# Performance work log

Hardware: AMD Instinct MI355X
Metric: run time of the kernel (lower is better)

## Reference

```python
import jax, jax.numpy as jnp
import numpy as np
from jax import lax

H = 64
IN = 3

def _lstm_layer(x, Wih, Whh, bih, bhh, collect):
    # x: [B, T, in]; Wih: [4H, in]; Whh: [4H, H]. PyTorch gate order: i, f, g, o.
    B = x.shape[0]
    h0 = jnp.zeros((B, H), x.dtype)
    c0 = jnp.zeros((B, H), x.dtype)
    b = bih + bhh
    def step(carry, xt):
        h, c = carry
        gates = xt @ Wih.T + h @ Whh.T + b  # [B, 4H]
        i, f, g, o = jnp.split(gates, 4, axis=-1)
        i = jax.nn.sigmoid(i); f = jax.nn.sigmoid(f)
        g = jnp.tanh(g); o = jax.nn.sigmoid(o)
        c = f * c + i * g
        h = o * jnp.tanh(c)
        return (h, c), (h if collect else None)
    xs = jnp.swapaxes(x, 0, 1)  # [T, B, in]
    (h, c), hs = lax.scan(step, (h0, c0), xs)
    if collect:
        return jnp.swapaxes(hs, 0, 1)  # [B, T, H]
    return h  # [B, H]


def setup_inputs() -> dict:
    key = jax.random.key(0)
    ks = jax.random.split(key, 14)
    s = 1.0 / np.sqrt(H)
    def u(k, shape):
        return jax.random.uniform(k, shape, jnp.float32, -s, s)
    return {
        "x": jax.random.normal(ks[0], (4096, 512, IN), jnp.float32),
        "Wih0": u(ks[1], (4 * H, IN)), "Whh0": u(ks[2], (4 * H, H)),
        "bih0": u(ks[3], (4 * H,)), "bhh0": u(ks[4], (4 * H,)),
        "Wih1": u(ks[5], (4 * H, H)), "Whh1": u(ks[6], (4 * H, H)),
        "bih1": u(ks[7], (4 * H,)), "bhh1": u(ks[8], (4 * H,)),
        "Wc1": jax.random.normal(ks[9], (32, H), jnp.float32) * 0.1,
        "bc1": jnp.zeros((32,), jnp.float32),
        "Wc2": jax.random.normal(ks[10], (1, 32), jnp.float32) * 0.1,
        "bc2": jnp.zeros((1,), jnp.float32),
    }


def reference(x, Wih0, Whh0, bih0, bhh0, Wih1, Whh1, bih1, bhh1, Wc1, bc1, Wc2, bc2):
    # 2-layer LSTM (dropout inactive at inference); only last timestep of layer 2 is used.
    h1 = _lstm_layer(x, Wih0, Whh0, bih0, bhh0, collect=True)   # [B, T, H]
    last = _lstm_layer(h1, Wih1, Whh1, bih1, bhh1, collect=False)  # [B, H]
    hidden = jax.nn.relu(last @ Wc1.T + bc1)  # [B, 32]
    out = jax.nn.sigmoid(hidden @ Wc2.T + bc2)  # [B, 1]
    return out
```

## Files before the change

### kernel.cpp

```cpp
#include <hip/hip_runtime.h>

#define TSEQ   512
#define BATCH  4096
#define MROWS  16

typedef short bf16x8 __attribute__((ext_vector_type(8)));
typedef short bf16x4 __attribute__((ext_vector_type(4)));
typedef float f32x4  __attribute__((ext_vector_type(4)));
typedef float f32x2  __attribute__((ext_vector_type(2)));
typedef unsigned int u32x2 __attribute__((ext_vector_type(2)));

#define NL2E  (-1.44269504f)
#define P2L2E (2.88539008f)

__device__ __forceinline__ unsigned short f2bf(float f) {
    unsigned int u = __builtin_bit_cast(unsigned int, f);
    return (unsigned short)((u + 0x8000u) >> 16);
}

__device__ __forceinline__ f32x2 cellupd2(const f32x4 a, const f32x4 b, f32x2& C) {
    f32x2 ei = {__builtin_amdgcn_exp2f(a[0]), __builtin_amdgcn_exp2f(b[0])};
    f32x2 ef = {__builtin_amdgcn_exp2f(a[1]), __builtin_amdgcn_exp2f(b[1])};
    f32x2 eg = {__builtin_amdgcn_exp2f(a[2]), __builtin_amdgcn_exp2f(b[2])};
    f32x2 eo = {__builtin_amdgcn_exp2f(a[3]), __builtin_amdgcn_exp2f(b[3])};
    f32x2 A  = 1.f + ei;
    f32x2 G1 = eg + 1.f;
    f32x2 F  = 1.f + ef;
    f32x2 t  = A * G1;
    f32x2 G2 = eg * P2L2E + (NL2E * 2.f);
    f32x2 num = C * t + G2 * F;
    f32x2 den = t * F;
    f32x2 r  = {__builtin_amdgcn_rcpf(den.x), __builtin_amdgcn_rcpf(den.y)};
    f32x2 Cn = num * r;
    Cn.x = fminf(Cn.x, 126.f);
    Cn.y = fminf(Cn.y, 126.f);
    C = Cn;
    f32x2 ec = {__builtin_amdgcn_exp2f(Cn.x), __builtin_amdgcn_exp2f(Cn.y)};
    f32x2 B  = 1.f + eo;
    f32x2 hn = ec - 1.f;
    f32x2 hd = B * (ec + 1.f);
    f32x2 rr = {__builtin_amdgcn_rcpf(hd.x), __builtin_amdgcn_rcpf(hd.y)};
    return hn * rr;
}


__global__ __launch_bounds__(512, 2) void lstm2_kernel(
    const float* __restrict__ x,
    const float* __restrict__ Wih0, const float* __restrict__ Whh0,
    const float* __restrict__ bih0, const float* __restrict__ bhh0,
    const float* __restrict__ Wih1, const float* __restrict__ Whh1,
    const float* __restrict__ bih1, const float* __restrict__ bhh1,
    const float* __restrict__ Wc1,  const float* __restrict__ bc1,
    const float* __restrict__ Wc2,  const float* __restrict__ bc2,
    float* __restrict__ out)
{
    __shared__ __align__(16) unsigned short ring[2][MROWS * 64];
    __shared__ __align__(16) unsigned short h2s[2][MROWS * 64];
    __shared__ __align__(16) unsigned short xq[64][128];
    __shared__ float h2f[MROWS][65];
    __shared__ float hid[MROWS][33];

    const int tid  = threadIdx.x;
    const int wv   = tid >> 6;
    const int lane = tid & 63;
    const int col  = lane & 15;
    const int lg   = lane >> 4;
    const int b0   = blockIdx.x * MROWS;
    const int sw   = (col & 7) << 4;

    for (int i = tid; i < 1024; i += 512) {
        ((unsigned int*)ring)[i] = 0u;
        ((unsigned int*)h2s)[i]  = 0u;
    }

    const int xrow = tid >> 5;
    const int xt   = tid & 31;
    const float* xb = x + ((size_t)(b0 + xrow) * TSEQ + xt) * 3;
    float xr0 = xb[0], xr1 = xb[1], xr2 = xb[2];
    {
        bf16x8 xf = {(short)f2bf(xr0),(short)f2bf(xr1),(short)f2bf(xr2),0,0,0,0,0};
        *(bf16x8*)((char*)xq + (xt << 8) + ((xrow << 4) ^ ((xt & 7) << 4))) = xf;
    }
    xr0 = xb[96]; xr1 = xb[97]; xr2 = xb[98];
    __syncthreads();

    const int rd0 = (col * 128 +      lg * 16) ^ sw;
    const int rd1 = (col * 128 + 64 + lg * 16) ^ sw;

#define FLUSH(S) do { \
    if (((S) & 31) == 16 && (S) < 480) { \
        const int c1_ = ((S) >> 5) + 1; \
        const int t64_ = ((c1_ & 1) << 5) + xt; \
        bf16x8 xf_ = {(short)f2bf(xr0),(short)f2bf(xr1),(short)f2bf(xr2),0,0,0,0,0}; \
        *(bf16x8*)((char*)xq + (t64_ << 8) + ((xrow << 4) ^ ((xt & 7) << 4))) = xf_; \
        if (c1_ < 15) { const float* p_ = xb + (c1_ + 1) * 96; xr0 = p_[0]; xr1 = p_[1]; xr2 = p_[2]; } \
    } \
} while(0)

    if (wv < 4) {
        const int wq = wv;
        const int ga = col & 3;
        const float sca = (ga == 2) ? P2L2E : NL2E;
        bf16x8 Wf[4][3];
        f32x4 bia4[4];
#pragma unroll
        for (int tt = 0; tt < 4; ++tt) {
            const int n = ga * 64 + 16 * (col >> 2) + 4 * wq + tt;
#pragma unroll
            for (int f = 0; f < 3; ++f)
#pragma unroll
                for (int i = 0; i < 8; ++i) {
                    const int k = f * 32 + lg * 8 + i;
                    float v = 0.f;
                    if (k < 64)      v = Whh0[n * 64 + k];
                    else if (k < 67) v = Wih0[n * 3 + (k - 64)];
                    Wf[tt][f][i] = (short)f2bf(sca * v);
                }
#pragma unroll
            for (int r = 0; r < 4; ++r) {
                const int nb = r * 64 + 16 * lg + 4 * wq + tt;
                bia4[tt][r] = ((r == 2) ? P2L2E : NL2E) * (bih0[nb] + bhh0[nb]);
            }
        }
        const int hw = (col * 128 + 32 * lg + 8 * wq) ^ sw;
        f32x2 C01 = {0.f, 0.f};
        f32x2 C23 = {0.f, 0.f};

#define L1B(RI, WI, S) do { \
        const char* rb_ = (const char*)ring[RI]; \
        bf16x8 v0_ = *(const bf16x8*)(rb_ + rd0); \
        bf16x8 v1_ = *(const bf16x8*)(rb_ + rd1); \
        bf16x8 v2_ = {0,0,0,0,0,0,0,0}; \
        if (lg == 0) \
            v2_ = *(const bf16x8*)((const char*)xq + ((((S)&63)) << 8) + ((col << 4) ^ (((S)&7) << 4))); \
        f32x4 a0_ = __builtin_amdgcn_mfma_f32_16x16x32_bf16(Wf[0][0], v0_, bia4[0],0,0,0); \
        f32x4 a1_ = __builtin_amdgcn_mfma_f32_16x16x32_bf16(Wf[1][0], v0_, bia4[1],0,0,0); \
        f32x4 a2_ = __builtin_amdgcn_mfma_f32_16x16x32_bf16(Wf[2][0], v0_, bia4[2],0,0,0); \
        f32x4 a3_ = __builtin_amdgcn_mfma_f32_16x16x32_bf16(Wf[3][0], v0_, bia4[3],0,0,0); \
        a0_ = __builtin_amdgcn_mfma_f32_16x16x32_bf16(Wf[0][1], v1_, a0_,0,0,0); \
        a1_ = __builtin_amdgcn_mfma_f32_16x16x32_bf16(Wf[1][1], v1_, a1_,0,0,0); \
        a2_ = __builtin_amdgcn_mfma_f32_16x16x32_bf16(Wf[2][1], v1_, a2_,0,0,0); \
        a3_ = __builtin_amdgcn_mfma_f32_16x16x32_bf16(Wf[3][1], v1_, a3_,0,0,0); \
        a0_ = __builtin_amdgcn_mfma_f32_16x16x32_bf16(Wf[0][2], v2_, a0_,0,0,0); \
        a1_ = __builtin_amdgcn_mfma_f32_16x16x32_bf16(Wf[1][2], v2_, a1_,0,0,0); \
        a2_ = __builtin_amdgcn_mfma_f32_16x16x32_bf16(Wf[2][2], v2_, a2_,0,0,0); \
        a3_ = __builtin_amdgcn_mfma_f32_16x16x32_bf16(Wf[3][2], v2_, a3_,0,0,0); \
        f32x2 h01_ = cellupd2(a0_, a1_, C01); \
        f32x2 h23_ = cellupd2(a2_, a3_, C23); \
        unsigned int p0_, p1_; \
        asm("v_cvt_pk_bf16_f32 %0, %1, %2" : "=v"(p0_) : "v"(h01_.x), "v"(h01_.y)); \
        asm("v_cvt_pk_bf16_f32 %0, %1, %2" : "=v"(p1_) : "v"(h23_.x), "v"(h23_.y)); \
        u32x2 pk_ = {p0_, p1_}; \
        *(u32x2*)((char*)ring[WI] + hw) = pk_; \
    } while(0)

        L1B(1, 0, 0);
        __syncthreads();
#pragma unroll 1
        for (int m = 0; m < 255; ++m) {
            const int s1 = 2 * m + 1;
            L1B(0, 1, s1);
            __syncthreads();
            L1B(1, 0, s1 + 1);
            FLUSH(s1 + 1);
            __syncthreads();
        }
        L1B(0, 1, 511);
        __syncthreads();
        __syncthreads();
#undef L1B
    } else {
        const int wq = wv - 4;
        const int ga = col & 3;
        const float sca = (ga == 2) ? P2L2E : NL2E;
        bf16x8 Wf[4][4];
        f32x4 bia4[4];
#pragma unroll
        for (int tt = 0; tt < 4; ++tt) {
            const int n = ga * 64 + 16 * (col >> 2) + 4 * wq + tt;
#pragma unroll
            for (int f = 0; f < 4; ++f)
#pragma unroll
                for (int i = 0; i < 8; ++i) {
                    const int k = f * 32 + lg * 8 + i;
                    const float v = (k < 64) ? Wih1[n * 64 + k] : Whh1[n * 64 + (k - 64)];
                    Wf[tt][f][i] = (short)f2bf(sca * v);
                }
#pragma unroll
            for (int r = 0; r < 4; ++r) {
                const int nb = r * 64 + 16 * lg + 4 * wq + tt;
                bia4[tt][r] = ((r == 2) ? P2L2E : NL2E) * (bih1[nb] + bhh1[nb]);
            }
        }
        const int hw2 = (col * 128 + 32 * lg + 8 * wq) ^ sw;
        f32x2 C01 = {0.f, 0.f};
        f32x2 C23 = {0.f, 0.f};
        f32x2 hv01 = {0.f, 0.f};
        f32x2 hv23 = {0.f, 0.f};

#define L2B(RB, HR) do { \
        const char* rb_ = (const char*)ring[RB]; \
        const char* hp_ = (const char*)h2s[HR]; \
        bf16x8 v0_ = *(const bf16x8*)(rb_ + rd0); \
        bf16x8 v1_ = *(const bf16x8*)(rb_ + rd1); \
        bf16x8 v2_ = *(const bf16x8*)(hp_ + rd0); \
        bf16x8 v3_ = *(const bf16x8*)(hp_ + rd1); \
        f32x4 a0_ = __builtin_amdgcn_mfma_f32_16x16x32_bf16(Wf[0][0], v0_, bia4[0],0,0,0); \
        f32x4 a1_ = __builtin_amdgcn_mfma_f32_16x16x32_bf16(Wf[1][0], v0_, bia4[1],0,0,0); \
        f32x4 a2_ = __builtin_amdgcn_mfma_f32_16x16x32_bf16(Wf[2][0], v0_, bia4[2],0,0,0); \
        f32x4 a3_ = __builtin_amdgcn_mfma_f32_16x16x32_bf16(Wf[3][0], v0_, bia4[3],0,0,0); \
        a0_ = __builtin_amdgcn_mfma_f32_16x16x32_bf16(Wf[0][1], v1_, a0_,0,0,0); \
        a1_ = __builtin_amdgcn_mfma_f32_16x16x32_bf16(Wf[1][1], v1_, a1_,0,0,0); \
        a2_ = __builtin_amdgcn_mfma_f32_16x16x32_bf16(Wf[2][1], v1_, a2_,0,0,0); \
        a3_ = __builtin_amdgcn_mfma_f32_16x16x32_bf16(Wf[3][1], v1_, a3_,0,0,0); \
        a0_ = __builtin_amdgcn_mfma_f32_16x16x32_bf16(Wf[0][2], v2_, a0_,0,0,0); \
        a1_ = __builtin_amdgcn_mfma_f32_16x16x32_bf16(Wf[1][2], v2_, a1_,0,0,0); \
        a2_ = __builtin_amdgcn_mfma_f32_16x16x32_bf16(Wf[2][2], v2_, a2_,0,0,0); \
        a3_ = __builtin_amdgcn_mfma_f32_16x16x32_bf16(Wf[3][2], v2_, a3_,0,0,0); \
        a0_ = __builtin_amdgcn_mfma_f32_16x16x32_bf16(Wf[0][3], v3_, a0_,0,0,0); \
        a1_ = __builtin_amdgcn_mfma_f32_16x16x32_bf16(Wf[1][3], v3_, a1_,0,0,0); \
        a2_ = __builtin_amdgcn_mfma_f32_16x16x32_bf16(Wf[2][3], v3_, a2_,0,0,0); \
        a3_ = __builtin_amdgcn_mfma_f32_16x16x32_bf16(Wf[3][3], v3_, a3_,0,0,0); \
        hv01 = cellupd2(a0_, a1_, C01); \
        hv23 = cellupd2(a2_, a3_, C23); \
        unsigned int p0_, p1_; \
        asm("v_cvt_pk_bf16_f32 %0, %1, %2" : "=v"(p0_) : "v"(hv01.x), "v"(hv01.y)); \
        asm("v_cvt_pk_bf16_f32 %0, %1, %2" : "=v"(p1_) : "v"(hv23.x), "v"(hv23.y)); \
        u32x2 pk_ = {p0_, p1_}; \
        *(u32x2*)((char*)h2s[RB] + hw2) = pk_; \
    } while(0)

        __syncthreads();
#pragma unroll 1
        for (int m = 0; m < 255; ++m) {
            L2B(0, 1);
            __syncthreads();
            L2B(1, 0);
            FLUSH(2 * m + 2);
            __syncthreads();
        }
        L2B(0, 1);
        __syncthreads();
        L2B(1, 0);
        __syncthreads();
#undef L2B
        const int ub = 16 * lg + 4 * wq;
        h2f[col][ub + 0] = hv01.x;
        h2f[col][ub + 1] = hv01.y;
        h2f[col][ub + 2] = hv23.x;
        h2f[col][ub + 3] = hv23.y;
    }
    __syncthreads();

    {
        const int b = tid & 15, j = tid >> 4;
        float s = bc1[j];
#pragma unroll 8
        for (int k = 0; k < 64; ++k) s += Wc1[j * 64 + k] * h2f[b][k];
        hid[b][j] = fmaxf(s, 0.f);
    }
    __syncthreads();
    if (tid < 16) {
        float s = bc2[0];
#pragma unroll 8
        for (int k = 0; k < 32; ++k) s += Wc2[k] * hid[tid][k];
        float e = __builtin_amdgcn_exp2f(NL2E * s);
        out[b0 + tid] = __builtin_amdgcn_rcpf(1.f + e);
    }
}

extern "C" void kernel_launch(void* const* d_in, const int* in_sizes, int n_in,
                              void* d_out, int out_size, void* d_ws, size_t ws_size,
                              hipStream_t stream) {
    lstm2_kernel<<<BATCH / MROWS, 512, 0, stream>>>(
        (const float*)d_in[0],
        (const float*)d_in[1], (const float*)d_in[2],
        (const float*)d_in[3], (const float*)d_in[4],
        (const float*)d_in[5], (const float*)d_in[6],
        (const float*)d_in[7], (const float*)d_in[8],
        (const float*)d_in[9], (const float*)d_in[10],
        (const float*)d_in[11], (const float*)d_in[12],
        (float*)d_out);
}
```

Before: 309.3 us.

## Split each LSTM layer across eight waves with two gate tiles each

```diff
diff --git a/kernel.cpp b/kernel.cpp
--- a/kernel.cpp
+++ b/kernel.cpp
@@ -8,7 +8,6 @@
 typedef short bf16x4 __attribute__((ext_vector_type(4)));
 typedef float f32x4  __attribute__((ext_vector_type(4)));
 typedef float f32x2  __attribute__((ext_vector_type(2)));
-typedef unsigned int u32x2 __attribute__((ext_vector_type(2)));
 
 #define NL2E  (-1.44269504f)
 #define P2L2E (2.88539008f)
@@ -44,7 +43,7 @@
 }
 
 
-__global__ __launch_bounds__(512, 2) void lstm2_kernel(
+__global__ __launch_bounds__(1024, 4) void lstm2_kernel(
     const float* __restrict__ x,
     const float* __restrict__ Wih0, const float* __restrict__ Whh0,
     const float* __restrict__ bih0, const float* __restrict__ bhh0,
@@ -68,20 +67,19 @@
     const int b0   = blockIdx.x * MROWS;
     const int sw   = (col & 7) << 4;
 
-    for (int i = tid; i < 1024; i += 512) {
-        ((unsigned int*)ring)[i] = 0u;
-        ((unsigned int*)h2s)[i]  = 0u;
-    }
-
-    const int xrow = tid >> 5;
+    ((unsigned int*)ring)[tid] = 0u;
+    ((unsigned int*)h2s)[tid]  = 0u;
+
+    const int xrow = (tid >> 5) & 15;
     const int xt   = tid & 31;
     const float* xb = x + ((size_t)(b0 + xrow) * TSEQ + xt) * 3;
-    float xr0 = xb[0], xr1 = xb[1], xr2 = xb[2];
-    {
+    float xr0 = 0.f, xr1 = 0.f, xr2 = 0.f;
+    if (tid < 512) {
+        xr0 = xb[0]; xr1 = xb[1]; xr2 = xb[2];
         bf16x8 xf = {(short)f2bf(xr0),(short)f2bf(xr1),(short)f2bf(xr2),0,0,0,0,0};
         *(bf16x8*)((char*)xq + (xt << 8) + ((xrow << 4) ^ ((xt & 7) << 4))) = xf;
-    }
-    xr0 = xb[96]; xr1 = xb[97]; xr2 = xb[98];
+        xr0 = xb[96]; xr1 = xb[97]; xr2 = xb[98];
+    }
     __syncthreads();
 
     const int rd0 = (col * 128 +      lg * 16) ^ sw;
@@ -97,15 +95,15 @@
     } \
 } while(0)
 
-    if (wv < 4) {
+    if (wv < 8) {
         const int wq = wv;
         const int ga = col & 3;
         const float sca = (ga == 2) ? P2L2E : NL2E;
-        bf16x8 Wf[4][3];
-        f32x4 bia4[4];
-#pragma unroll
-        for (int tt = 0; tt < 4; ++tt) {
-            const int n = ga * 64 + 16 * (col >> 2) + 4 * wq + tt;
+        bf16x8 Wf[2][3];
+        f32x4 bia4[2];
+#pragma unroll
+        for (int tt = 0; tt < 2; ++tt) {
+            const int n = ga * 64 + 16 * (col >> 2) + 2 * wq + tt;
 #pragma unroll
             for (int f = 0; f < 3; ++f)
 #pragma unroll
@@ -118,13 +116,12 @@
                 }
 #pragma unroll
             for (int r = 0; r < 4; ++r) {
-                const int nb = r * 64 + 16 * lg + 4 * wq + tt;
+                const int nb = r * 64 + 16 * lg + 2 * wq + tt;
                 bia4[tt][r] = ((r == 2) ? P2L2E : NL2E) * (bih0[nb] + bhh0[nb]);
             }
         }
-        const int hw = (col * 128 + 32 * lg + 8 * wq) ^ sw;
+        const int hw = (col * 128 + 32 * lg + 4 * wq) ^ sw;
         f32x2 C01 = {0.f, 0.f};
-        f32x2 C23 = {0.f, 0.f};
 
 #define L1B(RI, WI, S) do { \
         const char* rb_ = (const char*)ring[RI]; \
@@ -135,23 +132,14 @@
             v2_ = *(const bf16x8*)((const char*)xq + ((((S)&63)) << 8) + ((col << 4) ^ (((S)&7) << 4))); \
         f32x4 a0_ = __builtin_amdgcn_mfma_f32_16x16x32_bf16(Wf[0][0], v0_, bia4[0],0,0,0); \
         f32x4 a1_ = __builtin_amdgcn_mfma_f32_16x16x32_bf16(Wf[1][0], v0_, bia4[1],0,0,0); \
-        f32x4 a2_ = __builtin_amdgcn_mfma_f32_16x16x32_bf16(Wf[2][0], v0_, bia4[2],0,0,0); \
-        f32x4 a3_ = __builtin_amdgcn_mfma_f32_16x16x32_bf16(Wf[3][0], v0_, bia4[3],0,0,0); \
         a0_ = __builtin_amdgcn_mfma_f32_16x16x32_bf16(Wf[0][1], v1_, a0_,0,0,0); \
         a1_ = __builtin_amdgcn_mfma_f32_16x16x32_bf16(Wf[1][1], v1_, a1_,0,0,0); \
-        a2_ = __builtin_amdgcn_mfma_f32_16x16x32_bf16(Wf[2][1], v1_, a2_,0,0,0); \
-        a3_ = __builtin_amdgcn_mfma_f32_16x16x32_bf16(Wf[3][1], v1_, a3_,0,0,0); \
         a0_ = __builtin_amdgcn_mfma_f32_16x16x32_bf16(Wf[0][2], v2_, a0_,0,0,0); \
         a1_ = __builtin_amdgcn_mfma_f32_16x16x32_bf16(Wf[1][2], v2_, a1_,0,0,0); \
-        a2_ = __builtin_amdgcn_mfma_f32_16x16x32_bf16(Wf[2][2], v2_, a2_,0,0,0); \
-        a3_ = __builtin_amdgcn_mfma_f32_16x16x32_bf16(Wf[3][2], v2_, a3_,0,0,0); \
         f32x2 h01_ = cellupd2(a0_, a1_, C01); \
-        f32x2 h23_ = cellupd2(a2_, a3_, C23); \
-        unsigned int p0_, p1_; \
+        unsigned int p0_; \
         asm("v_cvt_pk_bf16_f32 %0, %1, %2" : "=v"(p0_) : "v"(h01_.x), "v"(h01_.y)); \
-        asm("v_cvt_pk_bf16_f32 %0, %1, %2" : "=v"(p1_) : "v"(h23_.x), "v"(h23_.y)); \
-        u32x2 pk_ = {p0_, p1_}; \
-        *(u32x2*)((char*)ring[WI] + hw) = pk_; \
+        *(unsigned int*)((char*)ring[WI] + hw) = p0_; \
     } while(0)
 
         L1B(1, 0, 0);
@@ -170,14 +158,14 @@
         __syncthreads();
 #undef L1B
     } else {
-        const int wq = wv - 4;
+        const int wq = wv - 8;
         const int ga = col & 3;
         const float sca = (ga == 2) ? P2L2E : NL2E;
-        bf16x8 Wf[4][4];
-        f32x4 bia4[4];
-#pragma unroll
-        for (int tt = 0; tt < 4; ++tt) {
-            const int n = ga * 64 + 16 * (col >> 2) + 4 * wq + tt;
+        bf16x8 Wf[2][4];
+        f32x4 bia4[2];
+#pragma unroll
+        for (int tt = 0; tt < 2; ++tt) {
+            const int n = ga * 64 + 16 * (col >> 2) + 2 * wq + tt;
 #pragma unroll
             for (int f = 0; f < 4; ++f)
 #pragma unroll
@@ -188,15 +176,13 @@
                 }
 #pragma unroll
             for (int r = 0; r < 4; ++r) {
-                const int nb = r * 64 + 16 * lg + 4 * wq + tt;
+                const int nb = r * 64 + 16 * lg + 2 * wq + tt;
                 bia4[tt][r] = ((r == 2) ? P2L2E : NL2E) * (bih1[nb] + bhh1[nb]);
             }
         }
-        const int hw2 = (col * 128 + 32 * lg + 8 * wq) ^ sw;
+        const int hw2 = (col * 128 + 32 * lg + 4 * wq) ^ sw;
         f32x2 C01 = {0.f, 0.f};
-        f32x2 C23 = {0.f, 0.f};
         f32x2 hv01 = {0.f, 0.f};
-        f32x2 hv23 = {0.f, 0.f};
 
 #define L2B(RB, HR) do { \
         const char* rb_ = (const char*)ring[RB]; \
@@ -207,27 +193,16 @@
         bf16x8 v3_ = *(const bf16x8*)(hp_ + rd1); \
         f32x4 a0_ = __builtin_amdgcn_mfma_f32_16x16x32_bf16(Wf[0][0], v0_, bia4[0],0,0,0); \
         f32x4 a1_ = __builtin_amdgcn_mfma_f32_16x16x32_bf16(Wf[1][0], v0_, bia4[1],0,0,0); \
-        f32x4 a2_ = __builtin_amdgcn_mfma_f32_16x16x32_bf16(Wf[2][0], v0_, bia4[2],0,0,0); \
-        f32x4 a3_ = __builtin_amdgcn_mfma_f32_16x16x32_bf16(Wf[3][0], v0_, bia4[3],0,0,0); \
         a0_ = __builtin_amdgcn_mfma_f32_16x16x32_bf16(Wf[0][1], v1_, a0_,0,0,0); \
         a1_ = __builtin_amdgcn_mfma_f32_16x16x32_bf16(Wf[1][1], v1_, a1_,0,0,0); \
-        a2_ = __builtin_amdgcn_mfma_f32_16x16x32_bf16(Wf[2][1], v1_, a2_,0,0,0); \
-        a3_ = __builtin_amdgcn_mfma_f32_16x16x32_bf16(Wf[3][1], v1_, a3_,0,0,0); \
         a0_ = __builtin_amdgcn_mfma_f32_16x16x32_bf16(Wf[0][2], v2_, a0_,0,0,0); \
         a1_ = __builtin_amdgcn_mfma_f32_16x16x32_bf16(Wf[1][2], v2_, a1_,0,0,0); \
-        a2_ = __builtin_amdgcn_mfma_f32_16x16x32_bf16(Wf[2][2], v2_, a2_,0,0,0); \
-        a3_ = __builtin_amdgcn_mfma_f32_16x16x32_bf16(Wf[3][2], v2_, a3_,0,0,0); \
         a0_ = __builtin_amdgcn_mfma_f32_16x16x32_bf16(Wf[0][3], v3_, a0_,0,0,0); \
         a1_ = __builtin_amdgcn_mfma_f32_16x16x32_bf16(Wf[1][3], v3_, a1_,0,0,0); \
-        a2_ = __builtin_amdgcn_mfma_f32_16x16x32_bf16(Wf[2][3], v3_, a2_,0,0,0); \
-        a3_ = __builtin_amdgcn_mfma_f32_16x16x32_bf16(Wf[3][3], v3_, a3_,0,0,0); \
         hv01 = cellupd2(a0_, a1_, C01); \
-        hv23 = cellupd2(a2_, a3_, C23); \
-        unsigned int p0_, p1_; \
+        unsigned int p0_; \
         asm("v_cvt_pk_bf16_f32 %0, %1, %2" : "=v"(p0_) : "v"(hv01.x), "v"(hv01.y)); \
-        asm("v_cvt_pk_bf16_f32 %0, %1, %2" : "=v"(p1_) : "v"(hv23.x), "v"(hv23.y)); \
-        u32x2 pk_ = {p0_, p1_}; \
-        *(u32x2*)((char*)h2s[RB] + hw2) = pk_; \
+        *(unsigned int*)((char*)h2s[RB] + hw2) = p0_; \
     } while(0)
 
         __syncthreads();
@@ -236,7 +211,6 @@
             L2B(0, 1);
             __syncthreads();
             L2B(1, 0);
-            FLUSH(2 * m + 2);
             __syncthreads();
         }
         L2B(0, 1);
@@ -244,15 +218,13 @@
         L2B(1, 0);
         __syncthreads();
 #undef L2B
-        const int ub = 16 * lg + 4 * wq;
+        const int ub = 16 * lg + 2 * wq;
         h2f[col][ub + 0] = hv01.x;
         h2f[col][ub + 1] = hv01.y;
-        h2f[col][ub + 2] = hv23.x;
-        h2f[col][ub + 3] = hv23.y;
     }
     __syncthreads();
 
-    {
+    if (tid < 512) {
         const int b = tid & 15, j = tid >> 4;
         float s = bc1[j];
 #pragma unroll 8
@@ -272,7 +244,7 @@
 extern "C" void kernel_launch(void* const* d_in, const int* in_sizes, int n_in,
                               void* d_out, int out_size, void* d_ws, size_t ws_size,
                               hipStream_t stream) {
-    lstm2_kernel<<<BATCH / MROWS, 512, 0, stream>>>(
+    lstm2_kernel<<<BATCH / MROWS, 1024, 0, stream>>>(
         (const float*)d_in[0],
         (const float*)d_in[1], (const float*)d_in[2],
         (const float*)d_in[3], (const float*)d_in[4],
```

Result: faster. 293.3 us (-5.2%).
